# Kernel tuning notes

Hardware: AMD Instinct MI355X
Metric: run time of the kernel (lower is better)

The kernel has to match this reference:

```python
import jax, jax.numpy as jnp
import numpy as np

HEADS = 4
KD = 32          # key_dim per head
LEVELS = 2
G = 3            # 2**dims - 1 HP orientation groups
STRENGTH = 0.25
DECAY = 0.6
LN_EPS = 1e-5
MIX_EPS = 1e-3


def _layernorm(x, g, b):
    m = jnp.mean(x, axis=-1, keepdims=True)
    v = jnp.var(x, axis=-1, keepdims=True)
    return (x - m) * jax.lax.rsqrt(v + LN_EPS) * g + b


def _dwt2(x):
    # Haar analysis, periodic/even sizes. [B,H,W,C] -> [B,H/2,W/2,4C] (LL,LH,HL,HH)
    x00 = x[:, 0::2, 0::2]; x01 = x[:, 0::2, 1::2]
    x10 = x[:, 1::2, 0::2]; x11 = x[:, 1::2, 1::2]
    ll = (x00 + x01 + x10 + x11) * 0.5
    lh = (x00 - x01 + x10 - x11) * 0.5
    hl = (x00 + x01 - x10 - x11) * 0.5
    hh = (x00 - x01 - x10 + x11) * 0.5
    return jnp.concatenate([ll, lh, hl, hh], axis=-1)


def _idwt2(w):
    # exact Haar synthesis: [B,H/2,W/2,4C] -> [B,H,W,C]
    ll, lh, hl, hh = jnp.split(w, 4, axis=-1)
    x00 = (ll + lh + hl + hh) * 0.5
    x01 = (ll - lh + hl - hh) * 0.5
    x10 = (ll + lh - hl - hh) * 0.5
    x11 = (ll - lh - hl + hh) * 0.5
    B, H2, W2, C = ll.shape
    r0 = jnp.stack([x00, x01], axis=3).reshape(B, H2, 2 * W2, C)  # interleave W
    r1 = jnp.stack([x10, x11], axis=3).reshape(B, H2, 2 * W2, C)
    return jnp.stack([r0, r1], axis=2).reshape(B, 2 * H2, 2 * W2, C)  # interleave H


def _axial_mhsa(x, p):
    # AxialMHSAND: sequential sweep over spatial axes; each pass is
    # proj(attn(softmax(QK^T/sqrt(d)) V)) on norm(x), qkv via 1x1 conv (=matmul).
    g, b, wq, bq, wk, bk, wv, bv, wp, bp = p
    scale = KD ** -0.5
    for axis in (1, 2):
        X = _layernorm(x, g, b)
        B, H, W, _ = X.shape
        Q = (X @ wq + bq).reshape(B, H, W, HEADS, KD)
        K = (X @ wk + bk).reshape(B, H, W, HEADS, KD)
        V = (X @ wv + bv).reshape(B, H, W, HEADS, KD)
        if axis == 1:  # attend along H, batch over (B, W, heads)
            A = jax.nn.softmax(jnp.einsum('bqwnd,bkwnd->bwnqk', Q, K) * scale, axis=-1)
            Y = jnp.einsum('bwnqk,bkwnd->bqwnd', A, V)
        else:          # attend along W, batch over (B, H, heads)
            A = jax.nn.softmax(jnp.einsum('bhqnd,bhknd->bhnqk', Q, K) * scale, axis=-1)
            Y = jnp.einsum('bhnqk,bhknd->bhqnd', A, V)
        x = Y.reshape(B, H, W, HEADS * KD) @ wp + bp
    return x


def setup_inputs() -> dict:
    key = jax.random.key(0)
    ks = jax.random.split(key, 24)
    C = 64
    HD = HEADS * KD
    s = 0.02
    inp = {'x': jax.random.normal(ks[0], (4, 256, 256, C), jnp.float32)}
    i = 1
    for pre in ('lp', 'hp'):
        inp[pre + '_ln_g'] = jnp.ones((C,), jnp.float32)
        inp[pre + '_ln_b'] = jnp.zeros((C,), jnp.float32)
        inp[pre + '_wq'] = jax.random.normal(ks[i], (C, HD), jnp.float32) * s
        inp[pre + '_bq'] = jax.random.normal(ks[i + 1], (HD,), jnp.float32) * s
        inp[pre + '_wk'] = jax.random.normal(ks[i + 2], (C, HD), jnp.float32) * s
        inp[pre + '_bk'] = jax.random.normal(ks[i + 3], (HD,), jnp.float32) * s
        inp[pre + '_wv'] = jax.random.normal(ks[i + 4], (C, HD), jnp.float32) * s
        inp[pre + '_bv'] = jax.random.normal(ks[i + 5], (HD,), jnp.float32) * s
        inp[pre + '_wp'] = jax.random.normal(ks[i + 6], (HD, C), jnp.float32) * s
        inp[pre + '_bp'] = jax.random.normal(ks[i + 7], (C,), jnp.float32) * s
        i += 8
    mix = jnp.eye(G, dtype=jnp.float32) + MIX_EPS * (jnp.ones((G, G), jnp.float32) - jnp.eye(G, dtype=jnp.float32))
    inp['mix_w0'] = mix
    inp['mix_w1'] = mix
    return inp


def reference(x, lp_ln_g, lp_ln_b, lp_wq, lp_bq, lp_wk, lp_bk, lp_wv, lp_bv, lp_wp, lp_bp,
              hp_ln_g, hp_ln_b, hp_wq, hp_bq, hp_wk, hp_bk, hp_wv, hp_bv, hp_wp, hp_bp,
              mix_w0, mix_w1):
    lp_p = (lp_ln_g, lp_ln_b, lp_wq, lp_bq, lp_wk, lp_bk, lp_wv, lp_bv, lp_wp, lp_bp)
    hp_p = (hp_ln_g, hp_ln_b, hp_wq, hp_bq, hp_wk, hp_bk, hp_wv, hp_bv, hp_wp, hp_bp)
    mix_ws = [mix_w0, mix_w1]
    C = x.shape[-1]
    cur = x
    hps = []
    for _ in range(LEVELS):  # analysis pyramid
        w = _dwt2(cur)
        hps.append(w[..., C:])
        cur = w[..., :C]
    # deepest LP: axial attention, residual with full strength
    cur = cur + STRENGTH * _axial_mhsa(cur, lp_p)
    for l in reversed(range(LEVELS)):  # synthesis with per-level HP processing
        hp = hps[l]
        B, H2, W2, _ = hp.shape
        gain = STRENGTH * (DECAY ** (LEVELS - 1 - l))  # coarser levels stronger
        hp_g = hp.reshape(B, H2, W2, G, C)
        mixed = jnp.einsum('gd,bhwdc->bhwgc', mix_ws[l], hp_g)  # OrientationMix
        batched = mixed.transpose(3, 0, 1, 2, 4).reshape(G * B, H2, W2, C)
        att = _axial_mhsa(batched, hp_p)  # shared hp_attn across groups/levels
        att = att.reshape(G, B, H2, W2, C).transpose(1, 2, 3, 0, 4).reshape(B, H2, W2, G * C)
        hp_out = hp + gain * att
        cur = _idwt2(jnp.concatenate([cur, hp_out], axis=-1))
    return cur
```

## Files before the change

kernel.cpp:

```cpp
#include <hip/hip_runtime.h>

#define LN_EPS 1e-5f
#define QSCALE 0.25500526578425445f

typedef __attribute__((ext_vector_type(8))) short bf16x8;
typedef __attribute__((ext_vector_type(4))) float f32x4;

#define MFMA16(A, B, C) __builtin_amdgcn_mfma_f32_16x16x32_bf16(A, B, C, 0, 0, 0)

static __device__ __forceinline__ unsigned short f2bf_rne(float f) {
    union { unsigned int i; float f; } c; c.f = f;
    unsigned int i = c.i;
    return (unsigned short)((i + 0x7fffu + ((i >> 16) & 1u)) >> 16);
}
static __device__ __forceinline__ void bfstore2(unsigned short* p, float x, float y) {
    *(unsigned int*)p = (unsigned int)f2bf_rne(x) | ((unsigned int)f2bf_rne(y) << 16);
}
static __device__ __forceinline__ unsigned pk2(float a, float b) {
    return __builtin_amdgcn_perm(__builtin_bit_cast(unsigned, b),
                                 __builtin_bit_cast(unsigned, a), 0x07060302u);
}
static __device__ __forceinline__ unsigned short tb16(float f) {
    return (unsigned short)(__builtin_bit_cast(unsigned, f) >> 16);
}

__global__ void dwt_kernel(const float4* __restrict__ in, float4* __restrict__ ll,
                           float4* __restrict__ hp, int B, int H2, int W2) {
    const int i = blockIdx.x * blockDim.x + threadIdx.x;
    const int total = B * H2 * W2 * 16;
    if (i >= total) return;
    const int c4 = i & 15;
    int t = i >> 4;
    const int w2 = t % W2; t /= W2;
    const int h2 = t % H2;
    const int b = t / H2;
    const int W = W2 * 2;
    const size_t base = (((size_t)b * (H2 * 2) + 2 * h2) * W + 2 * w2) * 16 + c4;
    const float4 x00 = in[base];
    const float4 x01 = in[base + 16];
    const float4 x10 = in[base + (size_t)W * 16];
    const float4 x11 = in[base + (size_t)W * 16 + 16];
    float4 vll, vlh, vhl, vhh;
#define DWTC(a) \
    vll.a = (x00.a + x01.a + x10.a + x11.a) * 0.5f; \
    vlh.a = (x00.a - x01.a + x10.a - x11.a) * 0.5f; \
    vhl.a = (x00.a + x01.a - x10.a - x11.a) * 0.5f; \
    vhh.a = (x00.a - x01.a - x10.a + x11.a) * 0.5f;
    DWTC(x) DWTC(y) DWTC(z) DWTC(w)
#undef DWTC
    const size_t oi = ((size_t)b * H2 + h2) * W2 + w2;
    ll[oi * 16 + c4] = vll;
    hp[oi * 48 + c4] = vlh;
    hp[oi * 48 + 16 + c4] = vhl;
    hp[oi * 48 + 32 + c4] = vhh;
}

__global__ void idwt_kernel(const float4* __restrict__ cur, const float4* __restrict__ hp,
                            const float4* __restrict__ att, float gain,
                            float4* __restrict__ out, int B, int H2, int W2) {
    const int i = blockIdx.x * blockDim.x + threadIdx.x;
    const int total = B * H2 * W2 * 16;
    if (i >= total) return;
    const int c4 = i & 15;
    int t = i >> 4;
    const int w2 = t % W2; t /= W2;
    const int h2 = t % H2;
    const int b = t / H2;
    const size_t oi = ((size_t)b * H2 + h2) * W2 + w2;
    const size_t sp = (size_t)h2 * W2 + w2;
    const size_t gstr = (size_t)B * H2 * W2;
    const float4 vll = cur[oi * 16 + c4];
    float4 vlh = hp[oi * 48 + c4];
    float4 vhl = hp[oi * 48 + 16 + c4];
    float4 vhh = hp[oi * 48 + 32 + c4];
    const float4 a0 = att[((size_t)b * H2 * W2 + sp) * 16 + c4];
    const float4 a1 = att[((size_t)b * H2 * W2 + gstr + sp) * 16 + c4];
    const float4 a2 = att[((size_t)b * H2 * W2 + 2 * gstr + sp) * 16 + c4];
#define ADDG(a) \
    vlh.a = fmaf(gain, a0.a, vlh.a); \
    vhl.a = fmaf(gain, a1.a, vhl.a); \
    vhh.a = fmaf(gain, a2.a, vhh.a);
    ADDG(x) ADDG(y) ADDG(z) ADDG(w)
#undef ADDG
    float4 x00, x01, x10, x11;
#define IDWTC(a) \
    x00.a = (vll.a + vlh.a + vhl.a + vhh.a) * 0.5f; \
    x01.a = (vll.a - vlh.a + vhl.a - vhh.a) * 0.5f; \
    x10.a = (vll.a + vlh.a - vhl.a - vhh.a) * 0.5f; \
    x11.a = (vll.a - vlh.a - vhl.a + vhh.a) * 0.5f;
    IDWTC(x) IDWTC(y) IDWTC(z) IDWTC(w)
#undef IDWTC
    const int W = W2 * 2;
    const size_t r0 = (((size_t)b * (H2 * 2) + 2 * h2) * W + 2 * w2) * 16 + c4;
    out[r0] = x00;
    out[r0 + 16] = x01;
    out[r0 + (size_t)W * 16] = x10;
    out[r0 + (size_t)W * 16 + 16] = x11;
}

__global__ void prep_weights(const float* __restrict__ lwq, const float* __restrict__ lwk,
                             const float* __restrict__ lwv, const float* __restrict__ lwp,
                             const float* __restrict__ hwq, const float* __restrict__ hwk,
                             const float* __restrict__ hwv, const float* __restrict__ hwp,
                             unsigned short* __restrict__ wbuf) {
    const int i = blockIdx.x * blockDim.x + threadIdx.x;
    if (i >= 65536) return;
    const int set = i >> 15;
    const int r = i & 32767;
    const float* wq = set ? hwq : lwq;
    const float* wk = set ? hwk : lwk;
    const float* wv = set ? hwv : lwv;
    const float* wp = set ? hwp : lwp;
    float v;
    if (r < 24576) {
        const int nn = r >> 6, c = r & 63;
        const float* w = (nn < 128) ? wq : (nn < 256) ? wk : wv;
        v = w[c * 128 + (nn & 127)];
        if (nn < 128) v *= QSCALE;
    } else {
        const int r2 = r - 24576;
        const int nn = r2 >> 7, d = r2 & 127;
        v = wp[d * 64 + nn];
    }
    wbuf[i] = f2bf_rne(v);
}

struct Job {
    const float* xin;
    const float* mixsrc;
    const float* mixw;
    float* xout;
    const float* basep;
    float res_scale;
    const float* ln_g; const float* ln_b;
    const float* bq; const float* bk; const float* bv; const float* bp;
    const unsigned short* wqkvT;
    const unsigned short* wpT;
};

template<int S>
__global__ __launch_bounds__(512, 4)
void axial_attn(Job jA, Job jB, int nA, int axis)
{
    constexpr int BS = 512;
    constexpr int NW = 8;
    constexpr int CK = 32;
    constexpr int NCH = S / CK;
    constexpr int CSTR = 40;
    constexpr int WPH = 2;
    constexpr int NSI = (S / 16) / WPH;

    __shared__ __align__(16) unsigned short Xs[S * 64];
    __shared__ __align__(16) unsigned short Qs[S * 128];
    __shared__ __align__(16) unsigned short Kc[CK * 128];
    __shared__ __align__(16) unsigned short Vc[128 * CSTR];
    __shared__ __align__(16) unsigned short Pb[NW * 16 * CSTR];

    const int tid = threadIdx.x;
    const int lane = tid & 63;
    const int w = tid >> 6;
    const int n16 = lane & 15;
    const int quad = lane >> 4;

    const bool isB = (int)blockIdx.x >= nA;
    const Job j = isB ? jB : jA;
    const int line = isB ? (int)blockIdx.x - nA : (int)blockIdx.x;
    const int lb = line / S;
    const int lr = line - lb * S;
    size_t lbase, tstr;
    if (axis == 1) { lbase = ((size_t)lb * S * S + lr) * 64; tstr = (size_t)S * 64; }
    else           { lbase = ((size_t)lb * S + lr) * (size_t)S * 64; tstr = 64; }

    {
        const int sub = tid & 15;
        const float4 g4 = ((const float4*)j.ln_g)[sub];
        const float4 be4 = ((const float4*)j.ln_b)[sub];
        const float4* x4 = (const float4*)j.xin;
        const float4* hp4 = (const float4*)j.mixsrc;
        const size_t lbase4 = lbase >> 2, tstr4 = tstr >> 2;
        float m0, m1, m2; int bimg;
        if (hp4) {
            const int g = lb >> 2;
            bimg = lb & 3;
            m0 = j.mixw[g * 3 + 0]; m1 = j.mixw[g * 3 + 1]; m2 = j.mixw[g * 3 + 2];
        }
        for (int t = (tid >> 4); t < S; t += BS / 16) {
            float4 v;
            if (hp4) {
                const int pos = (axis == 1) ? (t * S + lr) : (lr * S + t);
                const size_t hb = ((size_t)bimg * S * S + pos) * 48 + sub;
                const float4 h0 = hp4[hb];
                const float4 h1 = hp4[hb + 16];
                const float4 h2 = hp4[hb + 32];
                v.x = m0 * h0.x + m1 * h1.x + m2 * h2.x;
                v.y = m0 * h0.y + m1 * h1.y + m2 * h2.y;
                v.z = m0 * h0.z + m1 * h1.z + m2 * h2.z;
                v.w = m0 * h0.w + m1 * h1.w + m2 * h2.w;
            } else {
                v = x4[lbase4 + (size_t)t * tstr4 + sub];
            }
            float s = v.x + v.y + v.z + v.w;
            float ss = v.x * v.x + v.y * v.y + v.z * v.z + v.w * v.w;
            #pragma unroll
            for (int m = 1; m < 16; m <<= 1) {
                s += __shfl_xor(s, m);
                ss += __shfl_xor(ss, m);
            }
            const float mean = s * 0.015625f;
            const float rstd = rsqrtf(ss * 0.015625f - mean * mean + LN_EPS);
            unsigned short* xr = &Xs[(t << 6) + ((sub * 4) ^ ((t & 7) << 3))];
            bfstore2(xr,     (v.x - mean) * rstd * g4.x + be4.x,
                             (v.y - mean) * rstd * g4.y + be4.y);
            bfstore2(xr + 2, (v.z - mean) * rstd * g4.z + be4.z,
                             (v.w - mean) * rstd * g4.w + be4.w);
        }
    }
    __syncthreads();

    {
        const int nt = w;
        const int cbase = nt * 16;
        const float bias = j.bq[cbase + n16] * QSCALE;
        const bf16x8 Bf0 = *(const bf16x8*)&j.wqkvT[(nt * 16 + n16) * 64 + quad * 8];
        const bf16x8 Bf1 = *(const bf16x8*)&j.wqkvT[(nt * 16 + n16) * 64 + 32 + quad * 8];
        #pragma unroll
        for (int mt = 0; mt < S / 16; ++mt) {
            const int xr = mt * 16 + n16;
            const int xm = (xr & 7) << 3;
            const bf16x8 A0 = *(const bf16x8*)&Xs[(xr << 6) + ((quad * 8) ^ xm)];
            const bf16x8 A1 = *(const bf16x8*)&Xs[(xr << 6) + ((32 + quad * 8) ^ xm)];
            f32x4 acc = {bias, bias, bias, bias};
            acc = MFMA16(A0, Bf0, acc);
            acc = MFMA16(A1, Bf1, acc);
            const int row0 = mt * 16 + quad * 4;
            #pragma unroll
            for (int r = 0; r < 4; ++r) {
                const int rr = row0 + r;
                Qs[(rr << 7) + ((cbase + n16) ^ ((rr & 7) << 3))] = tb16(acc[r]);
            }
        }
    }
    __syncthreads();

    const int h = w >> 1;
    const int sub = w & 1;
    const int hoff = h * 32;
    unsigned short* pbw = &Pb[w * 16 * CSTR];
    const bf16x8 ones = (bf16x8)(short)0x3F80;

    bf16x8 qb[NSI];
    #pragma unroll
    for (int si = 0; si < NSI; ++si) {
        const int qr = (sub * NSI + si) * 16 + n16;
        qb[si] = *(const bf16x8*)&Qs[(qr << 7) + ((hoff + quad * 8) ^ ((qr & 7) << 3))];
    }
    f32x4 accl[NSI], y0[NSI], y1[NSI];
    #pragma unroll
    for (int si = 0; si < NSI; ++si) {
        accl[si] = (f32x4){0.f, 0.f, 0.f, 0.f};
        y0[si]   = (f32x4){0.f, 0.f, 0.f, 0.f};
        y1[si]   = (f32x4){0.f, 0.f, 0.f, 0.f};
    }

    for (int kc = 0; kc < NCH; ++kc) {
        const int k0 = kc * CK;
        #pragma unroll
        for (int i = 0; i < 4; ++i) {
            const int tix = w * 4 + i;
            const int region = tix >> 4;
            const int rem = tix & 15;
            const int nt = rem >> 1;
            const int mtl = rem & 1;
            const int wnt = 8 + region * 8 + nt;
            const bf16x8 W0 = *(const bf16x8*)&j.wqkvT[(wnt * 16 + n16) * 64 + quad * 8];
            const bf16x8 W1 = *(const bf16x8*)&j.wqkvT[(wnt * 16 + n16) * 64 + 32 + quad * 8];
            const float* bb = region ? j.bv : j.bk;
            const float bias = bb[nt * 16 + n16];
            const int xr = k0 + mtl * 16 + n16;
            const int xm = (xr & 7) << 3;
            const bf16x8 A0 = *(const bf16x8*)&Xs[(xr << 6) + ((quad * 8) ^ xm)];
            const bf16x8 A1 = *(const bf16x8*)&Xs[(xr << 6) + ((32 + quad * 8) ^ xm)];
            f32x4 acc = {bias, bias, bias, bias};
            acc = MFMA16(A0, W0, acc);
            acc = MFMA16(A1, W1, acc);
            if (region == 0) {
                const int row0 = mtl * 16 + quad * 4;
                #pragma unroll
                for (int r = 0; r < 4; ++r) {
                    const int rr = row0 + r;
                    Kc[(rr << 7) + ((nt * 16 + n16) ^ ((rr & 7) << 3))] = tb16(acc[r]);
                }
            } else {
                *(uint2*)&Vc[(nt * 16 + n16) * CSTR + mtl * 16 + quad * 4] =
                    make_uint2(pk2(acc[0], acc[1]), pk2(acc[2], acc[3]));
            }
        }
        __syncthreads();

        const bf16x8 vb0 = *(const bf16x8*)&Vc[(hoff + n16) * CSTR + quad * 8];
        const bf16x8 vb1 = *(const bf16x8*)&Vc[(hoff + 16 + n16) * CSTR + quad * 8];
        const int km = (n16 & 7) << 3;
        const bf16x8 ka0 = *(const bf16x8*)&Kc[(n16 << 7) + ((hoff + quad * 8) ^ km)];
        const bf16x8 ka1 = *(const bf16x8*)&Kc[((16 + n16) << 7) + ((hoff + quad * 8) ^ km)];
        #pragma unroll
        for (int si = 0; si < NSI; ++si) {
            f32x4 sc0 = {0.f, 0.f, 0.f, 0.f};
            f32x4 sc1 = {0.f, 0.f, 0.f, 0.f};
            sc0 = MFMA16(ka0, qb[si], sc0);
            sc1 = MFMA16(ka1, qb[si], sc1);
            *(uint2*)&pbw[n16 * CSTR + quad * 4] = make_uint2(
                pk2(__builtin_amdgcn_exp2f(sc0[0]), __builtin_amdgcn_exp2f(sc0[1])),
                pk2(__builtin_amdgcn_exp2f(sc0[2]), __builtin_amdgcn_exp2f(sc0[3])));
            *(uint2*)&pbw[n16 * CSTR + 16 + quad * 4] = make_uint2(
                pk2(__builtin_amdgcn_exp2f(sc1[0]), __builtin_amdgcn_exp2f(sc1[1])),
                pk2(__builtin_amdgcn_exp2f(sc1[2]), __builtin_amdgcn_exp2f(sc1[3])));
            const bf16x8 pa = *(const bf16x8*)&pbw[n16 * CSTR + quad * 8];
            accl[si] = MFMA16(pa, ones, accl[si]);
            y0[si] = MFMA16(pa, vb0, y0[si]);
            y1[si] = MFMA16(pa, vb1, y1[si]);
        }
        __syncthreads();
    }

    #pragma unroll
    for (int si = 0; si < NSI; ++si) {
        const int q0 = (sub * NSI + si) * 16;
        #pragma unroll
        for (int r = 0; r < 4; ++r) {
            const float inv = __builtin_amdgcn_rcpf(accl[si][r]);
            const int row = q0 + quad * 4 + r;
            const int m = (row & 7) << 3;
            Qs[(row << 7) + ((hoff + n16) ^ m)]      = tb16(y0[si][r] * inv);
            Qs[(row << 7) + ((hoff + 16 + n16) ^ m)] = tb16(y1[si][r] * inv);
        }
    }
    __syncthreads();

    {
        constexpr int TD = (S / 16) * 4 / NW;
        const int mt = (w * TD) >> 2;
        const int nt0 = (w * TD) & 3;
        const int m0 = mt * 16;
        const int ym = (n16 & 7) << 3;
        bf16x8 pa[4];
        #pragma unroll
        for (int kt = 0; kt < 4; ++kt)
            pa[kt] = *(const bf16x8*)&Qs[((m0 + n16) << 7) + ((kt * 32 + quad * 8) ^ ym)];
        #pragma unroll
        for (int i = 0; i < TD; ++i) {
            const int nt = nt0 + i;
            const float bias = j.bp[nt * 16 + n16];
            f32x4 acc = {bias, bias, bias, bias};
            #pragma unroll
            for (int kt = 0; kt < 4; ++kt) {
                const bf16x8 wb = *(const bf16x8*)&j.wpT[(nt * 16 + n16) * 128 + kt * 32 + quad * 8];
                acc = MFMA16(pa[kt], wb, acc);
            }
            #pragma unroll
            for (int r = 0; r < 4; ++r) {
                const size_t gi = lbase + (size_t)(m0 + quad * 4 + r) * tstr + nt * 16 + n16;
                float v = acc[r];
                if (j.basep) v = fmaf(j.res_scale, v, j.basep[gi]);
                j.xout[gi] = v;
            }
        }
    }
}

extern "C" void kernel_launch(void* const* d_in, const int* in_sizes, int n_in,
                              void* d_out, int out_size, void* d_ws, size_t ws_size,
                              hipStream_t stream) {
    (void)in_sizes; (void)n_in; (void)out_size; (void)ws_size;
    const float* x = (const float*)d_in[0];
    const float* P_lp[10];
    const float* P_hp[10];
    for (int i = 0; i < 10; ++i) P_lp[i] = (const float*)d_in[1 + i];
    for (int i = 0; i < 10; ++i) P_hp[i] = (const float*)d_in[11 + i];
    const float* mw0 = (const float*)d_in[21];
    const float* mw1 = (const float*)d_in[22];
    float* out = (float*)d_out;
    float* ws = (float*)d_ws;

    float* ll0 = ws;
    float* hp0 = ll0 + (size_t)4194304;
    float* t0  = hp0 + (size_t)12582912;
    float* ll1  = t0;
    float* hp1  = t0 + (size_t)1048576;
    float* ta2  = t0 + (size_t)4194304;
    float* lpta = t0 + (size_t)7340032;
    float* tb  = out;
    float* t1b = out;
    unsigned short* wbuf = (unsigned short*)(out + (size_t)13631488);

    prep_weights<<<256, 256, 0, stream>>>(
        P_lp[2], P_lp[4], P_lp[6], P_lp[8],
        P_hp[2], P_hp[4], P_hp[6], P_hp[8], wbuf);

    dwt_kernel<<<4 * 128 * 128 * 16 / 256, 256, 0, stream>>>(
        (const float4*)x, (float4*)ll0, (float4*)hp0, 4, 128, 128);
    dwt_kernel<<<4 * 64 * 64 * 16 / 256, 256, 0, stream>>>(
        (const float4*)ll0, (float4*)ll1, (float4*)hp1, 4, 64, 64);

    const unsigned short* lp_qkvT = wbuf;
    const unsigned short* lp_wpT  = wbuf + 24576;
    const unsigned short* hp_qkvT = wbuf + 32768;
    const unsigned short* hp_wpT  = wbuf + 32768 + 24576;

    auto mkjob = [](const float* xin, const float* mixsrc, const float* mixw,
                    float* xout, const float* basep, float rs,
                    const float* const* P, const unsigned short* qkvT,
                    const unsigned short* wpT) {
        Job jj;
        jj.xin = xin; jj.mixsrc = mixsrc; jj.mixw = mixw;
        jj.xout = xout; jj.basep = basep; jj.res_scale = rs;
        jj.ln_g = P[0]; jj.ln_b = P[1];
        jj.bq = P[3]; jj.bk = P[5]; jj.bv = P[7]; jj.bp = P[9];
        jj.wqkvT = qkvT; jj.wpT = wpT;
        return jj;
    };

    {
        Job a1 = mkjob(ll1, nullptr, nullptr, lpta, nullptr, 1.f, P_lp, lp_qkvT, lp_wpT);
        Job b1 = mkjob(nullptr, hp1, mw1, tb, nullptr, 1.f, P_hp, hp_qkvT, hp_wpT);
        axial_attn<64><<<1024, 512, 0, stream>>>(a1, b1, 256, 1);
        Job a2 = mkjob(lpta, nullptr, nullptr, ll1, ll1, 0.25f, P_lp, lp_qkvT, lp_wpT);
        Job b2 = mkjob(tb, nullptr, nullptr, ta2, nullptr, 1.f, P_hp, hp_qkvT, hp_wpT);
        axial_attn<64><<<1024, 512, 0, stream>>>(a2, b2, 256, 2);
    }
    idwt_kernel<<<4 * 64 * 64 * 16 / 256, 256, 0, stream>>>(
        (const float4*)ll1, (const float4*)hp1, (const float4*)ta2, 0.25f,
        (float4*)ll0, 4, 64, 64);

    {
        Job c1 = mkjob(nullptr, hp0, mw0, t1b, nullptr, 1.f, P_hp, hp_qkvT, hp_wpT);
        axial_attn<128><<<1536, 512, 0, stream>>>(c1, c1, 1536, 1);
        Job c2 = mkjob(t1b, nullptr, nullptr, t0, nullptr, 1.f, P_hp, hp_qkvT, hp_wpT);
        axial_attn<128><<<1536, 512, 0, stream>>>(c2, c2, 1536, 2);
    }
    idwt_kernel<<<4 * 128 * 128 * 16 / 256, 256, 0, stream>>>(
        (const float4*)ll0, (const float4*)hp0, (const float4*)t0, 0.15f,
        (float4*)out, 4, 128, 128);
}
```

Baseline: 452.8 us.

## Double-buffer K/V chunks, hoist K/V weights, replace ones-MFMA row sums

The K/V projection for the next key chunk is computed into a second LDS buffer while the current chunk is consumed. This cuts the per-chunk barrier count from two to one. K and V weights and biases are loaded into registers once per wave instead of being refetched every chunk. The softmax denominator now comes from scalar sums of the bf16-truncated exponentials, reduced with shuffles, instead of an extra MFMA against a ones vector. To fit the double buffers without raising LDS use, the Q buffer and the K/V buffers share one arena, which requires an extra barrier after Q is read into registers.

```diff
diff --git a/kernel.cpp b/kernel.cpp
--- a/kernel.cpp
+++ b/kernel.cpp
@@ -22,6 +22,9 @@
 }
 static __device__ __forceinline__ unsigned short tb16(float f) {
     return (unsigned short)(__builtin_bit_cast(unsigned, f) >> 16);
+}
+static __device__ __forceinline__ float bftrunc(float f) {
+    return __builtin_bit_cast(float, __builtin_bit_cast(unsigned, f) & 0xFFFF0000u);
 }
 
 __global__ void dwt_kernel(const float4* __restrict__ in, float4* __restrict__ ll,
@@ -146,14 +149,11 @@
     constexpr int NW = 8;
     constexpr int CK = 32;
     constexpr int NCH = S / CK;
+    constexpr int NSI = S / 32;
     constexpr int CSTR = 40;
-    constexpr int WPH = 2;
-    constexpr int NSI = (S / 16) / WPH;
 
     __shared__ __align__(16) unsigned short Xs[S * 64];
-    __shared__ __align__(16) unsigned short Qs[S * 128];
-    __shared__ __align__(16) unsigned short Kc[CK * 128];
-    __shared__ __align__(16) unsigned short Vc[128 * CSTR];
+    __shared__ __align__(16) unsigned short Arena[18432];
     __shared__ __align__(16) unsigned short Pb[NW * 16 * CSTR];
 
     const int tid = threadIdx.x;
@@ -170,6 +170,13 @@
     size_t lbase, tstr;
     if (axis == 1) { lbase = ((size_t)lb * S * S + lr) * 64; tstr = (size_t)S * 64; }
     else           { lbase = ((size_t)lb * S + lr) * (size_t)S * 64; tstr = 64; }
+
+    const bf16x8 Wk0 = *(const bf16x8*)&j.wqkvT[((8 + w) * 16 + n16) * 64 + quad * 8];
+    const bf16x8 Wk1 = *(const bf16x8*)&j.wqkvT[((8 + w) * 16 + n16) * 64 + 32 + quad * 8];
+    const bf16x8 Wv0 = *(const bf16x8*)&j.wqkvT[((16 + w) * 16 + n16) * 64 + quad * 8];
+    const bf16x8 Wv1 = *(const bf16x8*)&j.wqkvT[((16 + w) * 16 + n16) * 64 + 32 + quad * 8];
+    const float bk = j.bk[w * 16 + n16];
+    const float bv = j.bv[w * 16 + n16];
 
     {
         const int sub = tid & 15;
@@ -218,11 +225,9 @@
     __syncthreads();
 
     {
-        const int nt = w;
-        const int cbase = nt * 16;
-        const float bias = j.bq[cbase + n16] * QSCALE;
-        const bf16x8 Bf0 = *(const bf16x8*)&j.wqkvT[(nt * 16 + n16) * 64 + quad * 8];
-        const bf16x8 Bf1 = *(const bf16x8*)&j.wqkvT[(nt * 16 + n16) * 64 + 32 + quad * 8];
+        const float bias = j.bq[w * 16 + n16] * QSCALE;
+        const bf16x8 Bq0 = *(const bf16x8*)&j.wqkvT[(w * 16 + n16) * 64 + quad * 8];
+        const bf16x8 Bq1 = *(const bf16x8*)&j.wqkvT[(w * 16 + n16) * 64 + 32 + quad * 8];
         #pragma unroll
         for (int mt = 0; mt < S / 16; ++mt) {
             const int xr = mt * 16 + n16;
@@ -230,13 +235,13 @@
             const bf16x8 A0 = *(const bf16x8*)&Xs[(xr << 6) + ((quad * 8) ^ xm)];
             const bf16x8 A1 = *(const bf16x8*)&Xs[(xr << 6) + ((32 + quad * 8) ^ xm)];
             f32x4 acc = {bias, bias, bias, bias};
-            acc = MFMA16(A0, Bf0, acc);
-            acc = MFMA16(A1, Bf1, acc);
+            acc = MFMA16(A0, Bq0, acc);
+            acc = MFMA16(A1, Bq1, acc);
             const int row0 = mt * 16 + quad * 4;
             #pragma unroll
             for (int r = 0; r < 4; ++r) {
                 const int rr = row0 + r;
-                Qs[(rr << 7) + ((cbase + n16) ^ ((rr & 7) << 3))] = tb16(acc[r]);
+                Arena[(rr << 7) + ((w * 16 + n16) ^ ((rr & 7) << 3))] = tb16(acc[r]);
             }
         }
     }
@@ -246,92 +251,104 @@
     const int sub = w & 1;
     const int hoff = h * 32;
     unsigned short* pbw = &Pb[w * 16 * CSTR];
-    const bf16x8 ones = (bf16x8)(short)0x3F80;
 
     bf16x8 qb[NSI];
     #pragma unroll
     for (int si = 0; si < NSI; ++si) {
         const int qr = (sub * NSI + si) * 16 + n16;
-        qb[si] = *(const bf16x8*)&Qs[(qr << 7) + ((hoff + quad * 8) ^ ((qr & 7) << 3))];
-    }
-    f32x4 accl[NSI], y0[NSI], y1[NSI];
+        qb[si] = *(const bf16x8*)&Arena[(qr << 7) + ((hoff + quad * 8) ^ ((qr & 7) << 3))];
+    }
+    f32x4 y0[NSI], y1[NSI];
+    float rsum[NSI];
     #pragma unroll
     for (int si = 0; si < NSI; ++si) {
-        accl[si] = (f32x4){0.f, 0.f, 0.f, 0.f};
-        y0[si]   = (f32x4){0.f, 0.f, 0.f, 0.f};
-        y1[si]   = (f32x4){0.f, 0.f, 0.f, 0.f};
-    }
-
-    for (int kc = 0; kc < NCH; ++kc) {
+        y0[si] = (f32x4){0.f, 0.f, 0.f, 0.f};
+        y1[si] = (f32x4){0.f, 0.f, 0.f, 0.f};
+        rsum[si] = 0.f;
+    }
+    __syncthreads();
+
+    auto produce = [&](int kc, int buf) {
         const int k0 = kc * CK;
-        #pragma unroll
-        for (int i = 0; i < 4; ++i) {
-            const int tix = w * 4 + i;
-            const int region = tix >> 4;
-            const int rem = tix & 15;
-            const int nt = rem >> 1;
-            const int mtl = rem & 1;
-            const int wnt = 8 + region * 8 + nt;
-            const bf16x8 W0 = *(const bf16x8*)&j.wqkvT[(wnt * 16 + n16) * 64 + quad * 8];
-            const bf16x8 W1 = *(const bf16x8*)&j.wqkvT[(wnt * 16 + n16) * 64 + 32 + quad * 8];
-            const float* bb = region ? j.bv : j.bk;
-            const float bias = bb[nt * 16 + n16];
+        unsigned short* Kc = &Arena[buf * 4096];
+        unsigned short* Vc = &Arena[8192 + buf * 5120];
+        #pragma unroll
+        for (int mtl = 0; mtl < 2; ++mtl) {
             const int xr = k0 + mtl * 16 + n16;
             const int xm = (xr & 7) << 3;
             const bf16x8 A0 = *(const bf16x8*)&Xs[(xr << 6) + ((quad * 8) ^ xm)];
             const bf16x8 A1 = *(const bf16x8*)&Xs[(xr << 6) + ((32 + quad * 8) ^ xm)];
-            f32x4 acc = {bias, bias, bias, bias};
-            acc = MFMA16(A0, W0, acc);
-            acc = MFMA16(A1, W1, acc);
-            if (region == 0) {
-                const int row0 = mtl * 16 + quad * 4;
-                #pragma unroll
-                for (int r = 0; r < 4; ++r) {
-                    const int rr = row0 + r;
-                    Kc[(rr << 7) + ((nt * 16 + n16) ^ ((rr & 7) << 3))] = tb16(acc[r]);
-                }
-            } else {
-                *(uint2*)&Vc[(nt * 16 + n16) * CSTR + mtl * 16 + quad * 4] =
-                    make_uint2(pk2(acc[0], acc[1]), pk2(acc[2], acc[3]));
-            }
-        }
-        __syncthreads();
-
-        const bf16x8 vb0 = *(const bf16x8*)&Vc[(hoff + n16) * CSTR + quad * 8];
-        const bf16x8 vb1 = *(const bf16x8*)&Vc[(hoff + 16 + n16) * CSTR + quad * 8];
+            f32x4 ak = {bk, bk, bk, bk};
+            ak = MFMA16(A0, Wk0, ak);
+            ak = MFMA16(A1, Wk1, ak);
+            const int row0 = mtl * 16 + quad * 4;
+            #pragma unroll
+            for (int r = 0; r < 4; ++r) {
+                const int rr = row0 + r;
+                Kc[(rr << 7) + ((w * 16 + n16) ^ ((rr & 7) << 3))] = tb16(ak[r]);
+            }
+            f32x4 av = {bv, bv, bv, bv};
+            av = MFMA16(A0, Wv0, av);
+            av = MFMA16(A1, Wv1, av);
+            *(uint2*)&Vc[(w * 16 + n16) * CSTR + mtl * 16 + quad * 4] =
+                make_uint2(pk2(av[0], av[1]), pk2(av[2], av[3]));
+        }
+    };
+    auto consume = [&](int buf) {
+        const unsigned short* Kc = &Arena[buf * 4096];
+        const unsigned short* Vc = &Arena[8192 + buf * 5120];
         const int km = (n16 & 7) << 3;
         const bf16x8 ka0 = *(const bf16x8*)&Kc[(n16 << 7) + ((hoff + quad * 8) ^ km)];
         const bf16x8 ka1 = *(const bf16x8*)&Kc[((16 + n16) << 7) + ((hoff + quad * 8) ^ km)];
+        const bf16x8 vb0 = *(const bf16x8*)&Vc[(hoff + n16) * CSTR + quad * 8];
+        const bf16x8 vb1 = *(const bf16x8*)&Vc[(hoff + 16 + n16) * CSTR + quad * 8];
         #pragma unroll
         for (int si = 0; si < NSI; ++si) {
             f32x4 sc0 = {0.f, 0.f, 0.f, 0.f};
             f32x4 sc1 = {0.f, 0.f, 0.f, 0.f};
             sc0 = MFMA16(ka0, qb[si], sc0);
             sc1 = MFMA16(ka1, qb[si], sc1);
-            *(uint2*)&pbw[n16 * CSTR + quad * 4] = make_uint2(
-                pk2(__builtin_amdgcn_exp2f(sc0[0]), __builtin_amdgcn_exp2f(sc0[1])),
-                pk2(__builtin_amdgcn_exp2f(sc0[2]), __builtin_amdgcn_exp2f(sc0[3])));
-            *(uint2*)&pbw[n16 * CSTR + 16 + quad * 4] = make_uint2(
-                pk2(__builtin_amdgcn_exp2f(sc1[0]), __builtin_amdgcn_exp2f(sc1[1])),
-                pk2(__builtin_amdgcn_exp2f(sc1[2]), __builtin_amdgcn_exp2f(sc1[3])));
+            const float e0 = __builtin_amdgcn_exp2f(sc0[0]);
+            const float e1 = __builtin_amdgcn_exp2f(sc0[1]);
+            const float e2 = __builtin_amdgcn_exp2f(sc0[2]);
+            const float e3 = __builtin_amdgcn_exp2f(sc0[3]);
+            const float e4 = __builtin_amdgcn_exp2f(sc1[0]);
+            const float e5 = __builtin_amdgcn_exp2f(sc1[1]);
+            const float e6 = __builtin_amdgcn_exp2f(sc1[2]);
+            const float e7 = __builtin_amdgcn_exp2f(sc1[3]);
+            rsum[si] += ((bftrunc(e0) + bftrunc(e1)) + (bftrunc(e2) + bftrunc(e3)))
+                      + ((bftrunc(e4) + bftrunc(e5)) + (bftrunc(e6) + bftrunc(e7)));
+            *(uint2*)&pbw[n16 * CSTR + quad * 4] =
+                make_uint2(pk2(e0, e1), pk2(e2, e3));
+            *(uint2*)&pbw[n16 * CSTR + 16 + quad * 4] =
+                make_uint2(pk2(e4, e5), pk2(e6, e7));
             const bf16x8 pa = *(const bf16x8*)&pbw[n16 * CSTR + quad * 8];
-            accl[si] = MFMA16(pa, ones, accl[si]);
             y0[si] = MFMA16(pa, vb0, y0[si]);
             y1[si] = MFMA16(pa, vb1, y1[si]);
         }
+    };
+
+    produce(0, 0);
+    __syncthreads();
+    for (int kc = 0; kc < NCH; ++kc) {
+        if (kc + 1 < NCH) produce(kc + 1, (kc + 1) & 1);
+        consume(kc & 1);
         __syncthreads();
     }
 
     #pragma unroll
     for (int si = 0; si < NSI; ++si) {
+        float red = rsum[si];
+        red += __shfl_xor(red, 16);
+        red += __shfl_xor(red, 32);
         const int q0 = (sub * NSI + si) * 16;
         #pragma unroll
         for (int r = 0; r < 4; ++r) {
-            const float inv = __builtin_amdgcn_rcpf(accl[si][r]);
+            const float inv = __builtin_amdgcn_rcpf(__shfl(red, quad * 4 + r));
             const int row = q0 + quad * 4 + r;
             const int m = (row & 7) << 3;
-            Qs[(row << 7) + ((hoff + n16) ^ m)]      = tb16(y0[si][r] * inv);
-            Qs[(row << 7) + ((hoff + 16 + n16) ^ m)] = tb16(y1[si][r] * inv);
+            Arena[(row << 7) + ((hoff + n16) ^ m)]      = tb16(y0[si][r] * inv);
+            Arena[(row << 7) + ((hoff + 16 + n16) ^ m)] = tb16(y1[si][r] * inv);
         }
     }
     __syncthreads();
@@ -345,7 +362,7 @@
         bf16x8 pa[4];
         #pragma unroll
         for (int kt = 0; kt < 4; ++kt)
-            pa[kt] = *(const bf16x8*)&Qs[((m0 + n16) << 7) + ((kt * 32 + quad * 8) ^ ym)];
+            pa[kt] = *(const bf16x8*)&Arena[((m0 + n16) << 7) + ((kt * 32 + quad * 8) ^ ym)];
         #pragma unroll
         for (int i = 0; i < TD; ++i) {
             const int nt = nt0 + i;
```

After: 394.0 us. -13.0%, faster.
